# Performance work log

Measured on AMD Instinct MI355X. Metric: run time of the kernel, lower is better.

## Reference

```python
import jax, jax.numpy as jnp
import numpy as np


def setup_inputs() -> dict:
    key = jax.random.key(0)
    k1, k2, k3, k4 = jax.random.split(key, 4)
    B, S, D_IN, D_OUT = 4, 4096, 2048, 2048
    x = jax.random.normal(k1, (B, S, D_IN), dtype=jnp.float32)
    weight = jax.random.normal(k2, (D_OUT, D_IN), dtype=jnp.float32) * 0.02
    scale_weight = jax.random.uniform(k3, (D_OUT,), dtype=jnp.float32, minval=0.5, maxval=1.5)
    bias = jax.random.normal(k4, (D_OUT,), dtype=jnp.float32) * 0.02
    return {"x": x, "weight": weight, "scale_weight": scale_weight, "bias": bias}


def reference(x, weight, scale_weight, bias):
    # FPScaledLinear.forward: cast weight to compute dtype, apply per-out-feature
    # scale (scale_weight viewed as [out, 1]), then F.linear(x, w, b).
    w = weight * scale_weight[:, None]            # [out, in]
    out = jnp.einsum('bsi,oi->bso', x, w) + bias  # [B, S, out]
    return out
```

## Files before the change

kernel.cpp:

```cpp
#include <hip/hip_runtime.h>

typedef __attribute__((ext_vector_type(8))) __bf16 bf16x8;
typedef __attribute__((ext_vector_type(4))) float f32x4;
typedef __attribute__((ext_vector_type(8))) unsigned short ushort8;
typedef const __attribute__((address_space(1))) unsigned int gq_t;
typedef __attribute__((address_space(3))) unsigned int lq_t;

__device__ __forceinline__ unsigned short f2bf(float f) {
  unsigned int u = __builtin_bit_cast(unsigned int, f);
  u += 0x7fffu + ((u >> 16) & 1u);
  return (unsigned short)(u >> 16);
}

__global__ void cvt_x_kernel(const float* __restrict__ x, ushort8* __restrict__ o, int n8) {
  int stride = gridDim.x * blockDim.x;
  for (int i = blockIdx.x * blockDim.x + threadIdx.x; i < n8; i += stride) {
    const float4* p = (const float4*)(x) + 2 * (size_t)i;
    float4 v0 = p[0], v1 = p[1];
    ushort8 r;
    r[0] = f2bf(v0.x); r[1] = f2bf(v0.y); r[2] = f2bf(v0.z); r[3] = f2bf(v0.w);
    r[4] = f2bf(v1.x); r[5] = f2bf(v1.y); r[6] = f2bf(v1.z); r[7] = f2bf(v1.w);
    o[i] = r;
  }
}

__global__ void cvt_w_kernel(const float* __restrict__ w, const float* __restrict__ scale,
                             ushort8* __restrict__ o, int n8, int k8) {
  int stride = gridDim.x * blockDim.x;
  for (int i = blockIdx.x * blockDim.x + threadIdx.x; i < n8; i += stride) {
    float s = scale[i / k8];
    const float4* p = (const float4*)(w) + 2 * (size_t)i;
    float4 v0 = p[0], v1 = p[1];
    ushort8 r;
    r[0] = f2bf(v0.x * s); r[1] = f2bf(v0.y * s); r[2] = f2bf(v0.z * s); r[3] = f2bf(v0.w * s);
    r[4] = f2bf(v1.x * s); r[5] = f2bf(v1.y * s); r[6] = f2bf(v1.z * s); r[7] = f2bf(v1.w * s);
    o[i] = r;
  }
}


#define FENCE asm volatile("" ::: "memory")
#define BARRIER do { FENCE; __builtin_amdgcn_s_barrier(); FENCE; } while (0)
#define WAITV4 asm volatile("s_waitcnt vmcnt(4)" ::: "memory")
#define WAITV0 asm volatile("s_waitcnt vmcnt(0)" ::: "memory")

#define QUAD(MH, NH)                                                                     \
  do {                                                                                   \
    __builtin_amdgcn_s_setprio(1);                                                       \
    _Pragma("unroll") for (int k = 0; k < 2; ++k) {                                      \
      _Pragma("unroll") for (int mm = 0; mm < 4; ++mm) {                                 \
        _Pragma("unroll") for (int nn = 0; nn < 2; ++nn) {                               \
          acc[(MH)*4 + mm][(NH)*2 + nn] = __builtin_amdgcn_mfma_f32_16x16x32_bf16(       \
              af[mm][k], bg[NH][nn][k], acc[(MH)*4 + mm][(NH)*2 + nn], 0, 0, 0);         \
        }                                                                                \
      }                                                                                  \
    }                                                                                    \
    __builtin_amdgcn_s_setprio(0);                                                       \
  } while (0)

__global__ __launch_bounds__(512, 2) void gemm256_8ph(
    const unsigned short* __restrict__ A, const unsigned short* __restrict__ B,
    const float* __restrict__ bias, float* __restrict__ C, int M, int N, int K) {
  extern __shared__ char lds[];

  const int nbn = N >> 8;
  const int nwg = (M >> 8) * nbn;
  int bid = blockIdx.x;
  if ((nwg & 7) == 0) {
    int q = nwg >> 3;
    bid = (bid & 7) * q + (bid >> 3);
  }
  const int bm = (bid / nbn) << 8;
  const int bn = (bid % nbn) << 8;

  const int tid = threadIdx.x;
  const int lane = tid & 63;
  const int wid = tid >> 6;
  const int wr = wid >> 2;
  const int wc = wid & 3;
  const int NT = K >> 6;

  const int colel = (((tid & 7) ^ ((tid >> 3) & 7)) << 3);
  const unsigned short* a_g0 = A + (size_t)(bm + (tid >> 3)) * K + colel;
  const unsigned short* b_g0 = B + (size_t)(bn + ((tid >> 8) << 6) + ((tid >> 3) & 31)) * K + colel;

  auto STAGE_A = [&](int t, int mh, int buf) {
    const unsigned short* s = a_g0 + (size_t)(mh * 64) * K + t * 64;
    char* d = lds + buf * 65536 + mh * 16384 + tid * 16;
    __builtin_amdgcn_global_load_lds((gq_t*)s, (lq_t*)d, 16, 0, 0);
    __builtin_amdgcn_global_load_lds((gq_t*)(s + (size_t)128 * K), (lq_t*)(d + 8192), 16, 0, 0);
  };
  auto STAGE_B = [&](int t, int nh, int buf) {
    const unsigned short* s = b_g0 + (size_t)(nh * 32) * K + t * 64;
    char* d = lds + buf * 65536 + 32768 + nh * 16384 + tid * 16;
    __builtin_amdgcn_global_load_lds((gq_t*)s, (lq_t*)d, 16, 0, 0);
    __builtin_amdgcn_global_load_lds((gq_t*)(s + (size_t)128 * K), (lq_t*)(d + 8192), 16, 0, 0);
  };

  const int i15 = lane & 15;
  const int qg = lane >> 4;
  const int swz = (lane & 7) << 4;
  const int colp0 = (qg << 4) ^ swz;
  const int colp1 = ((qg << 4) | 64) ^ swz;
  const int aoff = wr * 8192 + i15 * 128;
  const int boff = 32768 + wc * 4096 + i15 * 128;

  f32x4 acc[8][4];
#pragma unroll
  for (int m = 0; m < 8; ++m)
#pragma unroll
    for (int n = 0; n < 4; ++n) acc[m][n] = (f32x4){0.f, 0.f, 0.f, 0.f};

  bf16x8 af[4][2];
  bf16x8 bg[2][2][2];

  auto LDA = [&](const char* base, int mh) {
    const char* p = base + mh * 16384 + aoff;
#pragma unroll
    for (int mm = 0; mm < 4; ++mm) {
      af[mm][0] = *(const bf16x8*)(p + mm * 2048 + colp0);
      af[mm][1] = *(const bf16x8*)(p + mm * 2048 + colp1);
    }
  };
  auto LDB = [&](const char* base, int nh) {
    const char* p = base + nh * 16384 + boff;
#pragma unroll
    for (int nn = 0; nn < 2; ++nn) {
      bg[nh][nn][0] = *(const bf16x8*)(p + nn * 2048 + colp0);
      bg[nh][nn][1] = *(const bf16x8*)(p + nn * 2048 + colp1);
    }
  };

  STAGE_A(0, 0, 0); STAGE_A(0, 1, 0); STAGE_B(0, 0, 0); STAGE_B(0, 1, 0);
  STAGE_A(1, 1, 1); STAGE_B(1, 1, 1);
  WAITV4;
  BARRIER;

  for (int t = 0; t < NT; ++t) {
    const int cb = t & 1, ob = cb ^ 1;
    const char* cur = lds + cb * 65536;

    LDA(cur, 0);
    LDB(cur, 0);
    if (t + 1 < NT) STAGE_A(t + 1, 0, ob);
    BARRIER;
    QUAD(0, 0);
    BARRIER;

    LDB(cur, 1);
    if (t + 1 < NT) STAGE_B(t + 1, 0, ob);
    BARRIER;
    QUAD(0, 1);
    BARRIER;

    LDA(cur, 1);
    if (t + 2 < NT) STAGE_A(t + 2, 1, cb);
    BARRIER;
    QUAD(1, 1);
    BARRIER;

    if (t + 2 < NT) STAGE_B(t + 2, 1, cb);
    BARRIER;
    QUAD(1, 0);
    if (t == NT - 2) { WAITV0; } else { WAITV4; }
    BARRIER;
  }

  const int r0 = bm + wr * 128 + ((lane >> 4) << 2);
  const int c0 = bn + wc * 64 + (lane & 15);
  float bv[4];
#pragma unroll
  for (int n = 0; n < 4; ++n) bv[n] = bias[c0 + n * 16];
#pragma unroll
  for (int m = 0; m < 8; ++m) {
#pragma unroll
    for (int r = 0; r < 4; ++r) {
      float* crow = C + (size_t)(r0 + m * 16 + r) * N + c0;
#pragma unroll
      for (int n = 0; n < 4; ++n) crow[n * 16] = acc[m][n][r] + bv[n];
    }
  }
}

__global__ void gemm_fallback_kernel(const float* __restrict__ X, const float* __restrict__ W,
                                     const float* __restrict__ scale, const float* __restrict__ bias,
                                     float* __restrict__ out, int M, int N, int K) {
  __shared__ float as[64][33];
  __shared__ float bs[64][33];
  int tx = threadIdx.x & 15, ty = threadIdx.x >> 4;
  int brow = blockIdx.y * 64, bcol = blockIdx.x * 64;
  float acc[4][4] = {};
  for (int k0 = 0; k0 < K; k0 += 32) {
    int kw = (K - k0 < 32) ? (K - k0) : 32;
    for (int i = 0; i < 8; ++i) {
      int idx = (int)threadIdx.x + i * 256;
      int r = idx >> 5, c = idx & 31;
      int ga = brow + r, gb = bcol + r;
      as[r][c] = (ga < M && c < kw) ? X[(size_t)ga * K + k0 + c] : 0.f;
      bs[r][c] = (gb < N && c < kw) ? W[(size_t)gb * K + k0 + c] * scale[gb] : 0.f;
    }
    __syncthreads();
    for (int k = 0; k < 32; ++k)
#pragma unroll
      for (int i = 0; i < 4; ++i)
#pragma unroll
        for (int j = 0; j < 4; ++j)
          acc[i][j] += as[ty * 4 + i][k] * bs[tx * 4 + j][k];
    __syncthreads();
  }
  for (int i = 0; i < 4; ++i) {
    int r = brow + ty * 4 + i;
    if (r >= M) continue;
    for (int j = 0; j < 4; ++j) {
      int c = bcol + tx * 4 + j;
      if (c < N) out[(size_t)r * N + c] = acc[i][j] + bias[c];
    }
  }
}

extern "C" void kernel_launch(void* const* d_in, const int* in_sizes, int n_in,
                              void* d_out, int out_size, void* d_ws, size_t ws_size,
                              hipStream_t stream) {
  const float* x     = (const float*)d_in[0];
  const float* w     = (const float*)d_in[1];
  const float* scale = (const float*)d_in[2];
  const float* bias  = (const float*)d_in[3];
  float* out = (float*)d_out;

  const long N = in_sizes[2];
  const long K = in_sizes[1] / N;
  const long M = (long)in_sizes[0] / K;

  const size_t need = ((size_t)M * K + (size_t)N * K) * sizeof(unsigned short);
  const long NT = K / 64;
  const bool ok = (ws_size >= need) && (M % 256 == 0) && (N % 256 == 0) &&
                  (K % 64 == 0) && (NT >= 3);

  if (ok) {
    unsigned short* xa = (unsigned short*)d_ws;
    unsigned short* wb = xa + (size_t)M * K;
    cvt_x_kernel<<<2048, 256, 0, stream>>>(x, (ushort8*)xa, (int)((size_t)M * K / 8));
    cvt_w_kernel<<<1024, 256, 0, stream>>>(w, scale, (ushort8*)wb, (int)((size_t)N * K / 8), (int)(K / 8));

    (void)hipFuncSetAttribute((const void*)gemm256_8ph,
                              hipFuncAttributeMaxDynamicSharedMemorySize, 131072);
    int nwg = (int)((M / 256) * (N / 256));
    gemm256_8ph<<<nwg, 512, 131072, stream>>>(xa, wb, bias, out, (int)M, (int)N, (int)K);
  } else {
    dim3 grid((unsigned)((N + 63) / 64), (unsigned)((M + 63) / 64));
    gemm_fallback_kernel<<<grid, 256, 0, stream>>>(x, w, scale, bias, out, (int)M, (int)N, (int)K);
  }
}
```

Measured before the change: 173.6 us.

## Restructure GEMM pipeline: prefetch next B fragment, unroll by two, incremental pointers

Reorders the 8-phase GEMM main loop so that the first B fragment of the next tile is read from LDS at the end of the current tile, overlapping that read with the last MFMA quad. It also changes which LDS sub-buffers are staged at each phase, unrolls the K loop by two to use compile-time buffer indices, and replaces per-stage address arithmetic with incrementing global pointers. The aim is to cut LDS-read latency exposed at tile start and to reduce scalar address overhead. In exchange it needs K to be a multiple of 128, uses more registers, and the reordered staging needs the vmcnt waits to stay correct.

```diff
diff --git a/kernel.cpp b/kernel.cpp
--- a/kernel.cpp
+++ b/kernel.cpp
@@ -43,19 +43,51 @@
 #define BARRIER do { FENCE; __builtin_amdgcn_s_barrier(); FENCE; } while (0)
 #define WAITV4 asm volatile("s_waitcnt vmcnt(4)" ::: "memory")
 #define WAITV0 asm volatile("s_waitcnt vmcnt(0)" ::: "memory")
-
-#define QUAD(MH, NH)                                                                     \
+#define GL(p, d) __builtin_amdgcn_global_load_lds((gq_t*)(p), (lq_t*)(d), 16, 0, 0)
+
+#define QUAD(MH, BG, NHB)                                                                \
   do {                                                                                   \
     __builtin_amdgcn_s_setprio(1);                                                       \
-    _Pragma("unroll") for (int k = 0; k < 2; ++k) {                                      \
+    _Pragma("unroll") for (int k_ = 0; k_ < 2; ++k_) {                                   \
       _Pragma("unroll") for (int mm = 0; mm < 4; ++mm) {                                 \
         _Pragma("unroll") for (int nn = 0; nn < 2; ++nn) {                               \
-          acc[(MH)*4 + mm][(NH)*2 + nn] = __builtin_amdgcn_mfma_f32_16x16x32_bf16(       \
-              af[mm][k], bg[NH][nn][k], acc[(MH)*4 + mm][(NH)*2 + nn], 0, 0, 0);         \
+          acc[(MH)*4 + mm][(NHB)*2 + nn] = __builtin_amdgcn_mfma_f32_16x16x32_bf16(      \
+              af[mm][k_], BG[nn][k_], acc[(MH)*4 + mm][(NHB)*2 + nn], 0, 0, 0);          \
         }                                                                                \
       }                                                                                  \
     }                                                                                    \
     __builtin_amdgcn_s_setprio(0);                                                       \
+  } while (0)
+
+#define TILE_BODY(T, CB)                                                                 \
+  do {                                                                                   \
+    const int t_ = (T);                                                                  \
+    char* cur = lds + (CB) * 65536;                                                      \
+    char* oth = lds + (((CB) ^ 1)) * 65536;                                              \
+                           \
+    LDA(cur, 0);                                                                         \
+    if (t_ + 1 < NT) { GL(bP0lo, oth + 32768 + dstT);                                    \
+                       GL(bP0hi, oth + 32768 + 8192 + dstT); }                           \
+    BARRIER; QUAD(0, bg0, 0); BARRIER;                                                   \
+                                   \
+    LDB1(cur);                                                                           \
+    if (t_ + 1 < NT) { GL(aP1lo, oth + 16384 + dstT);                                    \
+                       GL(aP1hi, oth + 16384 + 8192 + dstT); }                           \
+    BARRIER; QUAD(0, bg1, 1); BARRIER;                                                   \
+                                   \
+    LDA(cur, 1);                                                                         \
+    if (t_ + 2 < NT) { GL(aP0lo, cur + dstT);                                            \
+                       GL(aP0hi, cur + 8192 + dstT); }                                   \
+    BARRIER; QUAD(1, bg1, 1); BARRIER;                                                   \
+        \
+    if (t_ + 2 < NT) { GL(bP1lo, cur + 49152 + dstT);                                    \
+                       GL(bP1hi, cur + 49152 + 8192 + dstT); }                           \
+    if (t_ == NT - 2) { WAITV0; } else { WAITV4; }                                       \
+    BARRIER; QUAD(1, bg0, 0);                                                            \
+    if (t_ + 1 < NT) LDB0(oth);                                                          \
+    BARRIER;                                                                             \
+    aP0lo += 64; aP0hi += 64; aP1lo += 64; aP1hi += 64;                                  \
+    bP0lo += 64; bP0hi += 64; bP1lo += 64; bP1hi += 64;                                  \
   } while (0)
 
 __global__ __launch_bounds__(512, 2) void gemm256_8ph(
@@ -79,23 +111,19 @@
   const int wr = wid >> 2;
   const int wc = wid & 3;
   const int NT = K >> 6;
+  const int dstT = tid * 16;
 
   const int colel = (((tid & 7) ^ ((tid >> 3) & 7)) << 3);
-  const unsigned short* a_g0 = A + (size_t)(bm + (tid >> 3)) * K + colel;
-  const unsigned short* b_g0 = B + (size_t)(bn + ((tid >> 8) << 6) + ((tid >> 3) & 31)) * K + colel;
-
-  auto STAGE_A = [&](int t, int mh, int buf) {
-    const unsigned short* s = a_g0 + (size_t)(mh * 64) * K + t * 64;
-    char* d = lds + buf * 65536 + mh * 16384 + tid * 16;
-    __builtin_amdgcn_global_load_lds((gq_t*)s, (lq_t*)d, 16, 0, 0);
-    __builtin_amdgcn_global_load_lds((gq_t*)(s + (size_t)128 * K), (lq_t*)(d + 8192), 16, 0, 0);
-  };
-  auto STAGE_B = [&](int t, int nh, int buf) {
-    const unsigned short* s = b_g0 + (size_t)(nh * 32) * K + t * 64;
-    char* d = lds + buf * 65536 + 32768 + nh * 16384 + tid * 16;
-    __builtin_amdgcn_global_load_lds((gq_t*)s, (lq_t*)d, 16, 0, 0);
-    __builtin_amdgcn_global_load_lds((gq_t*)(s + (size_t)128 * K), (lq_t*)(d + 8192), 16, 0, 0);
-  };
+  const unsigned short* aBase = A + (size_t)(bm + (tid >> 3)) * K + colel;
+  const unsigned short* bBase = B + (size_t)(bn + ((tid >> 8) << 6) + ((tid >> 3) & 31)) * K + colel;
+  const unsigned short* aP0lo = aBase;
+  const unsigned short* aP0hi = aBase + (size_t)128 * K;
+  const unsigned short* aP1lo = aBase + (size_t)64 * K;
+  const unsigned short* aP1hi = aBase + (size_t)192 * K;
+  const unsigned short* bP0lo = bBase;
+  const unsigned short* bP0hi = bBase + (size_t)128 * K;
+  const unsigned short* bP1lo = bBase + (size_t)32 * K;
+  const unsigned short* bP1hi = bBase + (size_t)160 * K;
 
   const int i15 = lane & 15;
   const int qg = lane >> 4;
@@ -112,7 +140,8 @@
     for (int n = 0; n < 4; ++n) acc[m][n] = (f32x4){0.f, 0.f, 0.f, 0.f};
 
   bf16x8 af[4][2];
-  bf16x8 bg[2][2][2];
+  bf16x8 bg0[2][2];
+  bf16x8 bg1[2][2];
 
   auto LDA = [&](const char* base, int mh) {
     const char* p = base + mh * 16384 + aoff;
@@ -122,48 +151,39 @@
       af[mm][1] = *(const bf16x8*)(p + mm * 2048 + colp1);
     }
   };
-  auto LDB = [&](const char* base, int nh) {
-    const char* p = base + nh * 16384 + boff;
+  auto LDB0 = [&](const char* base) {
+    const char* p = base + boff;
 #pragma unroll
     for (int nn = 0; nn < 2; ++nn) {
-      bg[nh][nn][0] = *(const bf16x8*)(p + nn * 2048 + colp0);
-      bg[nh][nn][1] = *(const bf16x8*)(p + nn * 2048 + colp1);
+      bg0[nn][0] = *(const bf16x8*)(p + nn * 2048 + colp0);
+      bg0[nn][1] = *(const bf16x8*)(p + nn * 2048 + colp1);
     }
   };
-
-  STAGE_A(0, 0, 0); STAGE_A(0, 1, 0); STAGE_B(0, 0, 0); STAGE_B(0, 1, 0);
-  STAGE_A(1, 1, 1); STAGE_B(1, 1, 1);
+  auto LDB1 = [&](const char* base) {
+    const char* p = base + 16384 + boff;
+#pragma unroll
+    for (int nn = 0; nn < 2; ++nn) {
+      bg1[nn][0] = *(const bf16x8*)(p + nn * 2048 + colp0);
+      bg1[nn][1] = *(const bf16x8*)(p + nn * 2048 + colp1);
+    }
+  };
+
+  GL(aP0lo, lds + dstT);                     GL(aP0hi, lds + 8192 + dstT);
+  GL(aP1lo, lds + 16384 + dstT);             GL(aP1hi, lds + 16384 + 8192 + dstT);
+  GL(bP0lo, lds + 32768 + dstT);             GL(bP0hi, lds + 32768 + 8192 + dstT);
+  GL(bP1lo, lds + 49152 + dstT);             GL(bP1hi, lds + 49152 + 8192 + dstT);
+  GL(aP0lo + 64, lds + 65536 + dstT);        GL(aP0hi + 64, lds + 65536 + 8192 + dstT);
+  GL(bP1lo + 64, lds + 65536 + 49152 + dstT);
+  GL(bP1hi + 64, lds + 65536 + 49152 + 8192 + dstT);
   WAITV4;
   BARRIER;
-
-  for (int t = 0; t < NT; ++t) {
-    const int cb = t & 1, ob = cb ^ 1;
-    const char* cur = lds + cb * 65536;
-
-    LDA(cur, 0);
-    LDB(cur, 0);
-    if (t + 1 < NT) STAGE_A(t + 1, 0, ob);
-    BARRIER;
-    QUAD(0, 0);
-    BARRIER;
-
-    LDB(cur, 1);
-    if (t + 1 < NT) STAGE_B(t + 1, 0, ob);
-    BARRIER;
-    QUAD(0, 1);
-    BARRIER;
-
-    LDA(cur, 1);
-    if (t + 2 < NT) STAGE_A(t + 2, 1, cb);
-    BARRIER;
-    QUAD(1, 1);
-    BARRIER;
-
-    if (t + 2 < NT) STAGE_B(t + 2, 1, cb);
-    BARRIER;
-    QUAD(1, 0);
-    if (t == NT - 2) { WAITV0; } else { WAITV4; }
-    BARRIER;
+  LDB0(lds);
+  bP0lo += 64;  bP0hi += 64;  aP1lo += 64;  aP1hi += 64;
+  aP0lo += 128; aP0hi += 128; bP1lo += 128; bP1hi += 128;
+
+  for (int t = 0; t < NT; t += 2) {
+    TILE_BODY(t, 0);
+    TILE_BODY(t + 1, 1);
   }
 
   const int r0 = bm + wr * 128 + ((lane >> 4) << 2);
@@ -234,7 +254,7 @@
   const size_t need = ((size_t)M * K + (size_t)N * K) * sizeof(unsigned short);
   const long NT = K / 64;
   const bool ok = (ws_size >= need) && (M % 256 == 0) && (N % 256 == 0) &&
-                  (K % 64 == 0) && (NT >= 3);
+                  (K % 128 == 0) && (NT >= 4);
 
   if (ok) {
     unsigned short* xa = (unsigned short*)d_ws;
```

Result: no change. 173.7 us (+0.0%).
